# Kernel tuning notes

Measured on AMD Instinct MI355X. Metric: run time of the kernel, lower is better.

## Reference

```python
import jax, jax.numpy as jnp
import numpy as np

H = W = 256          # input_img_height (square images)
N_NODES = 8          # camera graph nodes
N_EDGES = 64         # ~fully connected directed graph
FEAT = 1024          # edge_feat_dim
BN_EPS = 1e-5


def setup_inputs() -> dict:
    key = jax.random.key(0)
    ks = jax.random.split(key, 8)
    d = {}
    d["x"] = jax.random.normal(ks[0], (N_NODES, 3 * H * W), dtype=jnp.float32)
    d["edge_index"] = jax.random.randint(ks[1], (2, N_EDGES), 0, N_NODES)
    # ResNet stem params (conv1 replaced to take 6 channels)
    d["conv1_w"] = jax.random.normal(ks[2], (64, 6, 7, 7), dtype=jnp.float32) * 0.05
    d["bn_gamma"] = jnp.ones((64,), jnp.float32)
    d["bn_beta"] = jnp.zeros((64,), jnp.float32)
    d["bn_mean"] = jnp.zeros((64,), jnp.float32)
    d["bn_var"] = jnp.ones((64,), jnp.float32)
    d["fc_w"] = jax.random.normal(ks[3], (FEAT, 64), dtype=jnp.float32) * 0.05
    d["fc_b"] = jnp.zeros((FEAT,), jnp.float32)
    d["fc_xyz_w"] = jax.random.normal(ks[4], (3, FEAT), dtype=jnp.float32) * 0.05
    d["fc_xyz_b"] = jnp.zeros((3,), jnp.float32)
    d["fc_wpqr_w"] = jax.random.normal(ks[5], (3, FEAT), dtype=jnp.float32) * 0.05
    d["fc_wpqr_b"] = jnp.zeros((3,), jnp.float32)
    return d


def _edge_extractor(ef, conv1_w, bn_gamma, bn_beta, bn_mean, bn_var, fc_w, fc_b):
    # conv1: 6->64, 7x7, stride 2, pad 3, no bias
    y = jax.lax.conv_general_dilated(
        ef, conv1_w, window_strides=(2, 2), padding=[(3, 3), (3, 3)],
        dimension_numbers=("NCHW", "OIHW", "NCHW"))
    # BatchNorm (inference form with running stats), fused scale/shift
    scale = (bn_gamma * jax.lax.rsqrt(bn_var + BN_EPS))[None, :, None, None]
    shift = (bn_beta - bn_mean * bn_gamma * jax.lax.rsqrt(bn_var + BN_EPS))[None, :, None, None]
    y = jax.nn.relu(y * scale + shift)
    # maxpool 3x3 stride 2 pad 1
    y = jax.lax.reduce_window(y, -jnp.inf, jax.lax.max,
                              (1, 1, 3, 3), (1, 1, 2, 2),
                              [(0, 0), (0, 0), (1, 1), (1, 1)])
    # AdaptiveAvgPool2d(1) + fc to edge_feat_dim
    y = jnp.mean(y, axis=(2, 3))                     # [E, 64]
    return y @ fc_w.T + fc_b                         # [E, FEAT]


def reference(x, edge_index, conv1_w, bn_gamma, bn_beta, bn_mean, bn_var,
              fc_w, fc_b, fc_xyz_w, fc_xyz_b, fc_wpqr_w, fc_wpqr_b):
    imgs = x.reshape(N_NODES, 3, H, W)
    # compute_edge_features, vectorized: gather min/max node per edge, concat channels
    nmin = jnp.min(edge_index, axis=0)               # [E]
    nmax = jnp.max(edge_index, axis=0)               # [E]
    edge_feat = jnp.concatenate([imgs[nmin], imgs[nmax]], axis=1)  # [E, 6, H, W]
    ef = _edge_extractor(edge_feat, conv1_w, bn_gamma, bn_beta, bn_mean, bn_var, fc_w, fc_b)
    ef = jax.nn.relu(ef)
    # droprate == 0 -> no dropout
    xyz = ef @ fc_xyz_w.T + fc_xyz_b                 # [E, 3]
    wpqr = ef @ fc_wpqr_w.T + fc_wpqr_b              # [E, 3]
    full = jnp.concatenate([xyz, wpqr], axis=1)      # [E, 6]
    return (full[:N_NODES], full)
```

## Files before the change

kernel.cpp:

```cpp
#include <hip/hip_runtime.h>
#include <hip/hip_bf16.h>

#define N_NODES 8
#define N_EDGES 64
#define CO 64
#define OH 128
#define OW 128
#define FEAT 1024
#define BN_EPS 1e-5f

#define OFF_PARTIAL 0
#define OFF_A       151552
#define OFF_B       (151552 + 16777216)

#define RS_W 136

typedef short bf16x8 __attribute__((ext_vector_type(8)));
typedef float f32x4  __attribute__((ext_vector_type(4)));

__device__ __forceinline__ unsigned short f2bf(float f) {
    unsigned u = __float_as_uint(f);
    u += 0x7fffu + ((u >> 16) & 1u);
    return (unsigned short)(u >> 16);
}
__device__ __forceinline__ float blo(unsigned u) { return __uint_as_float(u << 16); }
__device__ __forceinline__ float bhi(unsigned u) { return __uint_as_float(u & 0xffff0000u); }

__global__ __launch_bounds__(512, 4) void conv_kernel(
        const float* __restrict__ x, const float* __restrict__ w,
        const float* __restrict__ gamma, const float* __restrict__ beta,
        const float* __restrict__ mean,  const float* __restrict__ var,
        unsigned short* __restrict__ A2, unsigned short* __restrict__ B2) {
    int bx  = blockIdx.x;
    int r16 = bx & 7;
    int idx = bx >> 3;
    int n   = idx >> 4;
    int oy  = (r16 << 4) + (idx & 15);
    int t   = threadIdx.x;

    __shared__ __align__(16) char smem[62208];
    uint4*    wl4  = (uint4*)smem;
    unsigned* rawu = (unsigned*)(smem + 49152);

    for (int k2 = t; k2 < 3072; k2 += 512) {
        int rr  = k2 >> 7;
        int chp = k2 & 127;
        int h   = chp >> 6, c = chp & 63;
        union { unsigned short s[8]; uint4 v; } pk;
        pk.v = make_uint4(0u, 0u, 0u, 0u);
        if (rr < 21) {
            int ci = (rr * 147) >> 10;
            int ky = rr - ci * 7;
            float sc = gamma[c] * rsqrtf(var[c] + BN_EPS);
            const float* wr = w + ((c * 6 + h * 3 + ci) * 7 + ky) * 7;
#pragma unroll
            for (int kx = 0; kx < 7; ++kx)
                pk.s[kx] = f2bf(wr[kx] * sc);
        }
        wl4[k2] = pk.v;
    }

    const float* img = x + (size_t)n * (3 * 256 * 256);
    for (int k = t; k < 24 * RS_W; k += 512) {
        int u  = k % RS_W;
        int rr = k / RS_W;
        unsigned val = 0u;
        if (rr < 21 && u < 131) {
            int ci = (rr * 147) >> 10;
            int ky = rr - ci * 7;
            int iy = 2 * oy - 3 + ky;
            if ((unsigned)iy < 256u) {
                int c0 = 2 * u - 3;
                const float* row = img + (ci * 256 + iy) * 256;
                float f0 = ((unsigned)c0 < 256u) ? row[c0] : 0.f;
                float f1 = ((unsigned)(c0 + 1) < 256u) ? row[c0 + 1] : 0.f;
                val = (unsigned)f2bf(f0) | ((unsigned)f2bf(f1) << 16);
            }
        }
        rawu[k] = val;
    }
    __syncthreads();

    int wv = t >> 6, lane = t & 63;
    int h  = wv & 1, wg = wv >> 1;
    int quad = lane >> 4, m = lane & 15;

    f32x4 acc[4][2];
#pragma unroll
    for (int ct = 0; ct < 4; ++ct) {
        acc[ct][0] = (f32x4){0.f, 0.f, 0.f, 0.f};
        acc[ct][1] = (f32x4){0.f, 0.f, 0.f, 0.f};
    }

    const bf16x8* wlv = (const bf16x8*)smem;

#pragma unroll 2
    for (int s = 0; s < 6; ++s) {
        int rq = 4 * s + quad;
        bf16x8 afrag[2];
#pragma unroll
        for (int nt = 0; nt < 2; ++nt) {
            int ox = 32 * wg + 16 * nt + m;
            int base = rq * RS_W + ox;
            union { unsigned u[4]; bf16x8 v; } bb;
            bb.u[0] = rawu[base];     bb.u[1] = rawu[base + 1];
            bb.u[2] = rawu[base + 2]; bb.u[3] = rawu[base + 3];
            afrag[nt] = bb.v;
        }
#pragma unroll
        for (int ct = 0; ct < 4; ++ct) {
            bf16x8 wfrag = wlv[rq * 128 + h * 64 + 16 * ct + m];
#pragma unroll
            for (int nt = 0; nt < 2; ++nt)
                acc[ct][nt] = __builtin_amdgcn_mfma_f32_16x16x32_bf16(
                                  afrag[nt], wfrag, acc[ct][nt], 0, 0, 0);
        }
    }

    float sh[4] = {0.f, 0.f, 0.f, 0.f};
    if (h) {
#pragma unroll
        for (int ct = 0; ct < 4; ++ct) {
            int c = 16 * ct + m;
            float sc = gamma[c] * rsqrtf(var[c] + BN_EPS);
            sh[ct] = beta[c] - mean[c] * sc;
        }
    }

    __syncthreads();
    unsigned short* T = (unsigned short*)smem;

#pragma unroll
    for (int ct = 0; ct < 4; ++ct) {
        int chp = h * 64 + 16 * ct + m;
        int sw  = (chp & 7) << 2;
#pragma unroll
        for (int nt = 0; nt < 2; ++nt) {
            int px0 = 32 * wg + 16 * nt + 4 * quad;
            float v0 = acc[ct][nt][0] + sh[ct];
            float v1 = acc[ct][nt][1] + sh[ct];
            float v2 = acc[ct][nt][2] + sh[ct];
            float v3 = acc[ct][nt][3] + sh[ct];
            uint2 pk;
            pk.x = (unsigned)f2bf(v0) | ((unsigned)f2bf(v1) << 16);
            pk.y = (unsigned)f2bf(v2) | ((unsigned)f2bf(v3) << 16);
            int gs = ((px0 >> 2) ^ sw);
            *(uint2*)&T[chp * 128 + gs * 4] = pk;
        }
    }
    __syncthreads();

    int row = t >> 2, slot = t & 3;
    int hh = row >> 6, ch = row & 63;
    int swr = (row & 7) << 2;
    unsigned short* dst = (hh ? B2 : A2)
                        + ((size_t)(n * CO + ch) << 14) + (oy << 7) + slot * 32;
#pragma unroll
    for (int i = 0; i < 4; ++i) {
        int g  = slot * 8 + i * 2;
        int gs = g ^ swr;
        *(uint4*)(dst + i * 8) = *(uint4*)&T[row * 128 + gs * 4];
    }
}

__global__ __launch_bounds__(256, 4) void pool_kernel(
        const unsigned short* __restrict__ A2,
        const unsigned short* __restrict__ B2,
        float* __restrict__ partial) {
    int pb  = blockIdx.x;
    int xcd = pb & 7;
    int q   = pb >> 3;
    int c   = q >> 1;
    int rt  = xcd * 2 + (q & 1);
    int t   = threadIdx.x;

    __shared__ unsigned short S[2 * 8 * 9 * 128];

    for (int k = t; k < 2304; k += 256) {
        int slot = k & 15;
        int r    = (k >> 4) % 9;
        int tn   = (k >> 4) / 9;
        int grow = 8 * rt - 1 + r;
        uint4 v = make_uint4(0u, 0u, 0u, 0u);
        if (grow >= 0) {
            const unsigned short* src = (tn >= 8) ? B2 : A2;
            int node = tn & 7;
            v = *(const uint4*)(src + ((size_t)(node * CO + c) << 14)
                                    + (grow << 7) + slot * 8);
        }
        *(uint4*)&S[tn * 1152 + (r << 7) + slot * 8] = v;
    }
    __syncthreads();

    int wv = t >> 6, lane = t & 63;
    int esub = lane >> 4, tc = lane & 15;

    for (int i = 0; i < 3; ++i) {
        int sidx = 12 * wv + 4 * i + esub;
        bool valid = sidx < 36;
        int ss = valid ? sidx : 0;
        int pi = 0, rem = ss;
        while (rem >= 8 - pi) { rem -= 8 - pi; ++pi; }
        int pj = pi + rem;
        const unsigned short* pa  = &S[pi * 1152];
        const unsigned short* pb2 = &S[(8 + pj) * 1152];

        float mx[4][4];
#pragma unroll
        for (int p = 0; p < 4; ++p)
#pragma unroll
            for (int qq = 0; qq < 4; ++qq) mx[p][qq] = 0.f;

#pragma unroll
        for (int r = 0; r < 9; ++r) {
            uint4 ga = *(const uint4*)(pa + (r << 7) + tc * 8);
            uint4 gb = *(const uint4*)(pb2 + (r << 7) + tc * 8);
            float ha = 0.f, hb = 0.f;
            if (tc > 0) {
                ha = bhi(*(const unsigned*)(pa + (r << 7) + tc * 8 - 2));
                hb = bhi(*(const unsigned*)(pb2 + (r << 7) + tc * 8 - 2));
            }
            float z0 = ha + hb;
            float z1 = blo(ga.x) + blo(gb.x), z2 = bhi(ga.x) + bhi(gb.x);
            float z3 = blo(ga.y) + blo(gb.y), z4 = bhi(ga.y) + bhi(gb.y);
            float z5 = blo(ga.z) + blo(gb.z), z6 = bhi(ga.z) + bhi(gb.z);
            float z7 = blo(ga.w) + blo(gb.w), z8 = bhi(ga.w) + bhi(gb.w);
            float h0 = fmaxf(fmaxf(z0, z1), z2);
            float h1 = fmaxf(fmaxf(z2, z3), z4);
            float h2 = fmaxf(fmaxf(z4, z5), z6);
            float h3 = fmaxf(fmaxf(z6, z7), z8);
            if (r & 1) {
                int p = (r - 1) >> 1;
                mx[p][0] = fmaxf(mx[p][0], h0); mx[p][1] = fmaxf(mx[p][1], h1);
                mx[p][2] = fmaxf(mx[p][2], h2); mx[p][3] = fmaxf(mx[p][3], h3);
            } else {
                if (r >= 2) {
                    int p = (r >> 1) - 1;
                    mx[p][0] = fmaxf(mx[p][0], h0); mx[p][1] = fmaxf(mx[p][1], h1);
                    mx[p][2] = fmaxf(mx[p][2], h2); mx[p][3] = fmaxf(mx[p][3], h3);
                }
                if (r <= 6) {
                    int p = r >> 1;
                    mx[p][0] = fmaxf(mx[p][0], h0); mx[p][1] = fmaxf(mx[p][1], h1);
                    mx[p][2] = fmaxf(mx[p][2], h2); mx[p][3] = fmaxf(mx[p][3], h3);
                }
            }
        }

        float sum = 0.f;
#pragma unroll
        for (int p = 0; p < 4; ++p)
#pragma unroll
            for (int qq = 0; qq < 4; ++qq) sum += fmaxf(mx[p][qq], 0.f);

        sum += __shfl_down(sum, 8, 64);
        sum += __shfl_down(sum, 4, 64);
        sum += __shfl_down(sum, 2, 64);
        sum += __shfl_down(sum, 1, 64);
        if (tc == 0 && valid)
            partial[(rt * 36 + sidx) * 64 + c] = sum;
    }
}

__global__ __launch_bounds__(256) void head_kernel(
        const int* __restrict__ ei, const float* __restrict__ partial,
        const float* __restrict__ fc_w,   const float* __restrict__ fc_b,
        const float* __restrict__ xyz_w,  const float* __restrict__ xyz_b,
        const float* __restrict__ wpqr_w, const float* __restrict__ wpqr_b,
        float* __restrict__ out) {
    int e = blockIdx.x;
    int t = threadIdx.x;
    int a0 = ei[e], a1 = ei[N_EDGES + e];
    int pi = min(a0, a1), pj = max(a0, a1);
    int rank = pi * 8 - ((pi * (pi + 1)) >> 1) + pj;
    __shared__ float pl[CO];
    if (t < CO) {
        float s = 0.f;
#pragma unroll
        for (int rt = 0; rt < 16; ++rt)
            s += partial[(rt * 36 + rank) * 64 + t];
        pl[t] = s * (1.f / 4096.f);
    }
    __syncthreads();

    float s[6] = {0.f, 0.f, 0.f, 0.f, 0.f, 0.f};
#pragma unroll
    for (int ff = 0; ff < 4; ++ff) {
        int f = ff * 256 + t;
        const float* wr = fc_w + f * CO;
        float d = fc_b[f];
#pragma unroll
        for (int c = 0; c < CO; ++c) d = fmaf(pl[c], wr[c], d);
        d = fmaxf(d, 0.f);
#pragma unroll
        for (int r = 0; r < 3; ++r) {
            s[r]     = fmaf(d, xyz_w[r * FEAT + f],  s[r]);
            s[3 + r] = fmaf(d, wpqr_w[r * FEAT + f], s[3 + r]);
        }
    }
#pragma unroll
    for (int r = 0; r < 6; ++r)
#pragma unroll
        for (int off = 32; off > 0; off >>= 1)
            s[r] += __shfl_down(s[r], off, 64);

    __shared__ float red[4][6];
    if ((t & 63) == 0) {
#pragma unroll
        for (int r = 0; r < 6; ++r) red[t >> 6][r] = s[r];
    }
    __syncthreads();
    if (t < 6) {
        float v = red[0][t] + red[1][t] + red[2][t] + red[3][t];
        v += (t < 3) ? xyz_b[t] : wpqr_b[t - 3];
        out[48 + e * 6 + t] = v;
        if (e < 8) out[e * 6 + t] = v;
    }
}

extern "C" void kernel_launch(void* const* d_in, const int* in_sizes, int n_in,
                              void* d_out, int out_size, void* d_ws, size_t ws_size,
                              hipStream_t stream) {
    const float* x        = (const float*)d_in[0];
    const int*   ei       = (const int*)d_in[1];
    const float* conv1_w  = (const float*)d_in[2];
    const float* bn_gamma = (const float*)d_in[3];
    const float* bn_beta  = (const float*)d_in[4];
    const float* bn_mean  = (const float*)d_in[5];
    const float* bn_var   = (const float*)d_in[6];
    const float* fc_w     = (const float*)d_in[7];
    const float* fc_b     = (const float*)d_in[8];
    const float* xyz_w    = (const float*)d_in[9];
    const float* xyz_b    = (const float*)d_in[10];
    const float* wpqr_w   = (const float*)d_in[11];
    const float* wpqr_b   = (const float*)d_in[12];
    float* out = (float*)d_out;

    char* ws = (char*)d_ws;
    float*          partial = (float*)(ws + OFF_PARTIAL);
    unsigned short* A2      = (unsigned short*)(ws + OFF_A);
    unsigned short* B2      = (unsigned short*)(ws + OFF_B);

    conv_kernel<<<1024, 512, 0, stream>>>(x, conv1_w, bn_gamma, bn_beta,
                                          bn_mean, bn_var, A2, B2);
    pool_kernel<<<1024, 256, 0, stream>>>(A2, B2, partial);
    head_kernel<<<64, 256, 0, stream>>>(ei, partial, fc_w, fc_b,
                                        xyz_w, xyz_b, wpqr_w, wpqr_b, out);
}
```

Baseline: 139.2 us.

## Precompute padded bf16 images and scaled weights in a prep kernel

Adds a prep kernel that converts the input images once into a zero-padded, pair-packed bf16 layout and folds the BN scale into bf16 conv weights stored in global memory. Each conv block then loads its input rows with 16-byte vector copies instead of converting fp32 scalars, and reads weight fragments straight from global/L2 instead of building them in shared memory. This removes the per-block conversion work that was repeated across 1024 blocks and halves shared memory use, which may raise occupancy. In exchange it adds an extra kernel launch, a global round trip for the padded images, and weight loads from cache inside the MFMA loop.

Result: faster. 135.3 us (-2.8%).

```diff
diff --git a/kernel.cpp b/kernel.cpp
--- a/kernel.cpp
+++ b/kernel.cpp
@@ -10,10 +10,13 @@
 #define BN_EPS 1e-5f
 
 #define OFF_PARTIAL 0
-#define OFF_A       151552
-#define OFF_B       (151552 + 16777216)
+#define OFF_XPAD    151552
+#define OFF_WB      3471616
+#define OFF_A       3520768
+#define OFF_B       20297984
 
 #define RS_W 136
+#define XROW 132
 
 typedef short bf16x8 __attribute__((ext_vector_type(8)));
 typedef float f32x4  __attribute__((ext_vector_type(4)));
@@ -26,8 +29,44 @@
 __device__ __forceinline__ float blo(unsigned u) { return __uint_as_float(u << 16); }
 __device__ __forceinline__ float bhi(unsigned u) { return __uint_as_float(u & 0xffff0000u); }
 
+__global__ __launch_bounds__(256) void prep_kernel(
+        const float* __restrict__ x, const float* __restrict__ w,
+        const float* __restrict__ gamma, const float* __restrict__ var,
+        unsigned* __restrict__ xpad, unsigned short* __restrict__ wb2) {
+    int idx = blockIdx.x * 256 + threadIdx.x;
+    if (idx < 8 * 3 * 262 * XROW) {
+        int u   = idx % XROW;
+        int r   = idx / XROW;
+        int iyp = r % 262;
+        int nc  = r / 262;
+        int iy  = iyp - 3;
+        unsigned val = 0u;
+        if ((unsigned)iy < 256u) {
+            int c0 = 2 * u - 3;
+            const float* row = x + (size_t)nc * 65536 + iy * 256;
+            float f0 = ((unsigned)c0 < 256u) ? row[c0] : 0.f;
+            float f1 = ((unsigned)(c0 + 1) < 256u) ? row[c0 + 1] : 0.f;
+            val = (unsigned)f2bf(f0) | ((unsigned)f2bf(f1) << 16);
+        }
+        xpad[idx] = val;
+    }
+    if (idx < 2 * 64 * 192) {
+        int tp = idx % 192;
+        int c  = (idx / 192) & 63;
+        int h  = idx / (192 * 64);
+        int rr = tp >> 3, kx = tp & 7;
+        float val = 0.f;
+        if (rr < 21 && kx < 7) {
+            int ci = rr / 7, ky = rr % 7;
+            float sc = gamma[c] * rsqrtf(var[c] + BN_EPS);
+            val = w[((c * 6 + h * 3 + ci) * 7 + ky) * 7 + kx] * sc;
+        }
+        wb2[(rr * 128 + h * 64 + c) * 8 + kx] = f2bf(val);
+    }
+}
+
 __global__ __launch_bounds__(512, 4) void conv_kernel(
-        const float* __restrict__ x, const float* __restrict__ w,
+        const unsigned* __restrict__ xpad, const unsigned short* __restrict__ wb2,
         const float* __restrict__ gamma, const float* __restrict__ beta,
         const float* __restrict__ mean,  const float* __restrict__ var,
         unsigned short* __restrict__ A2, unsigned short* __restrict__ B2) {
@@ -38,46 +77,20 @@
     int oy  = (r16 << 4) + (idx & 15);
     int t   = threadIdx.x;
 
-    __shared__ __align__(16) char smem[62208];
-    uint4*    wl4  = (uint4*)smem;
-    unsigned* rawu = (unsigned*)(smem + 49152);
-
-    for (int k2 = t; k2 < 3072; k2 += 512) {
-        int rr  = k2 >> 7;
-        int chp = k2 & 127;
-        int h   = chp >> 6, c = chp & 63;
-        union { unsigned short s[8]; uint4 v; } pk;
-        pk.v = make_uint4(0u, 0u, 0u, 0u);
-        if (rr < 21) {
+    __shared__ __align__(16) char smem[32768];
+    unsigned* rawu = (unsigned*)smem;
+
+    const unsigned* src = xpad + (size_t)n * (3 * 262 * XROW);
+    for (int k = t; k < 24 * 34; k += 512) {
+        int g  = k % 34;
+        int rr = k / 34;
+        uint4 v = make_uint4(0u, 0u, 0u, 0u);
+        if (rr < 21 && g < 33) {
             int ci = (rr * 147) >> 10;
             int ky = rr - ci * 7;
-            float sc = gamma[c] * rsqrtf(var[c] + BN_EPS);
-            const float* wr = w + ((c * 6 + h * 3 + ci) * 7 + ky) * 7;
-#pragma unroll
-            for (int kx = 0; kx < 7; ++kx)
-                pk.s[kx] = f2bf(wr[kx] * sc);
-        }
-        wl4[k2] = pk.v;
-    }
-
-    const float* img = x + (size_t)n * (3 * 256 * 256);
-    for (int k = t; k < 24 * RS_W; k += 512) {
-        int u  = k % RS_W;
-        int rr = k / RS_W;
-        unsigned val = 0u;
-        if (rr < 21 && u < 131) {
-            int ci = (rr * 147) >> 10;
-            int ky = rr - ci * 7;
-            int iy = 2 * oy - 3 + ky;
-            if ((unsigned)iy < 256u) {
-                int c0 = 2 * u - 3;
-                const float* row = img + (ci * 256 + iy) * 256;
-                float f0 = ((unsigned)c0 < 256u) ? row[c0] : 0.f;
-                float f1 = ((unsigned)(c0 + 1) < 256u) ? row[c0 + 1] : 0.f;
-                val = (unsigned)f2bf(f0) | ((unsigned)f2bf(f1) << 16);
-            }
-        }
-        rawu[k] = val;
+            v = *(const uint4*)(src + (ci * 262 + 2 * oy + ky) * XROW + 4 * g);
+        }
+        *(uint4*)&rawu[rr * RS_W + 4 * g] = v;
     }
     __syncthreads();
 
@@ -92,7 +105,7 @@
         acc[ct][1] = (f32x4){0.f, 0.f, 0.f, 0.f};
     }
 
-    const bf16x8* wlv = (const bf16x8*)smem;
+    const bf16x8* wbv = (const bf16x8*)wb2;
 
 #pragma unroll 2
     for (int s = 0; s < 6; ++s) {
@@ -109,7 +122,7 @@
         }
 #pragma unroll
         for (int ct = 0; ct < 4; ++ct) {
-            bf16x8 wfrag = wlv[rq * 128 + h * 64 + 16 * ct + m];
+            bf16x8 wfrag = wbv[rq * 128 + h * 64 + 16 * ct + m];
 #pragma unroll
             for (int nt = 0; nt < 2; ++nt)
                 acc[ct][nt] = __builtin_amdgcn_mfma_f32_16x16x32_bf16(
@@ -338,10 +351,15 @@
 
     char* ws = (char*)d_ws;
     float*          partial = (float*)(ws + OFF_PARTIAL);
+    unsigned*       xpad    = (unsigned*)(ws + OFF_XPAD);
+    unsigned short* wb2     = (unsigned short*)(ws + OFF_WB);
     unsigned short* A2      = (unsigned short*)(ws + OFF_A);
     unsigned short* B2      = (unsigned short*)(ws + OFF_B);
 
-    conv_kernel<<<1024, 512, 0, stream>>>(x, conv1_w, bn_gamma, bn_beta,
+    int img_work = 8 * 3 * 262 * XROW;
+    prep_kernel<<<(img_work + 255) / 256, 256, 0, stream>>>(
+        x, conv1_w, bn_gamma, bn_var, xpad, wb2);
+    conv_kernel<<<1024, 512, 0, stream>>>(xpad, wb2, bn_gamma, bn_beta,
                                           bn_mean, bn_var, A2, B2);
     pool_kernel<<<1024, 256, 0, stream>>>(A2, B2, partial);
     head_kernel<<<64, 256, 0, stream>>>(ei, partial, fc_w, fc_b,
```
